# Performance work log

Hardware: AMD Instinct MI355X
Metric: run time of the kernel (lower is better)

Reference implementation:

```python
import jax, jax.numpy as jnp
import numpy as np

# Module dims (match init_kwargs)
D_IN = 1024
N_PRI = 2048
D_PRI = 16
N_CLS = 25
D_CLS = 16
ITERS = 3
B = 64
EPS = 1e-6


def layer_norm(x, g, b, eps=1e-5):
    m = x.mean(-1, keepdims=True)
    v = ((x - m) ** 2).mean(-1, keepdims=True)
    return (x - m) / jnp.sqrt(v + eps) * g + b


def setup_inputs() -> dict:
    key = jax.random.key(0)
    ks = jax.random.split(key, 6)
    s = lambda n: 1.0 / np.sqrt(n)
    return {
        "z": jax.random.normal(ks[0], (B, D_IN), jnp.float32),
        # to_primary: Linear(d_in, n_primary*d_primary)
        "w1": jax.random.normal(ks[1], (D_IN, N_PRI * D_PRI), jnp.float32) * s(D_IN),
        "b1": jnp.zeros((N_PRI * D_PRI,), jnp.float32),
        # primary_act: LayerNorm(d_in) -> Linear(d_in, n_primary) -> Sigmoid
        "ln1_g": jnp.ones((D_IN,), jnp.float32),
        "ln1_b": jnp.zeros((D_IN,), jnp.float32),
        "w2": jax.random.normal(ks[2], (D_IN, N_PRI), jnp.float32) * s(D_IN),
        "b2": jnp.zeros((N_PRI,), jnp.float32),
        # CapsuleFC transform + EM routing params
        "w_caps": jax.random.normal(ks[3], (N_PRI, D_PRI, N_CLS, D_CLS), jnp.float32) * s(D_PRI),
        "beta_u": jnp.zeros((N_CLS,), jnp.float32),
        "beta_a": jnp.zeros((N_CLS,), jnp.float32),
        # to_logits: LayerNorm(d_class) -> Linear(d_class, 1)
        "ln2_g": jnp.ones((D_CLS,), jnp.float32),
        "ln2_b": jnp.zeros((D_CLS,), jnp.float32),
        "w3": jax.random.normal(ks[4], (D_CLS, 1), jnp.float32) * s(D_CLS),
        "b3": jnp.zeros((1,), jnp.float32),
    }


def em_routing(V, a_in, beta_u, beta_a, n_iter):
    # V: (b, n_in, n_out, d) votes; a_in: (b, n_in) primary activations
    b, n, o, d = V.shape
    R = jnp.full((b, n, o), 1.0 / o, V.dtype)  # routing assignments
    lam = jnp.asarray(1.0, V.dtype)            # inverse temperature
    for _ in range(n_iter):
        # M-step: weighted mean/variance per output capsule
        r = R * a_in[:, :, None]                                  # (b,n,o)
        r_sum = r.sum(axis=1) + EPS                               # (b,o)
        mu = jnp.einsum('bno,bnod->bod', r, V) / r_sum[..., None]  # (b,o,d)
        diff2 = (V - mu[:, None]) ** 2                            # (b,n,o,d)
        sigma2 = jnp.einsum('bno,bnod->bod', r, diff2) / r_sum[..., None] + EPS
        cost = (beta_u[None, :, None] + 0.5 * jnp.log(sigma2)) * r_sum[..., None]
        a_out = jax.nn.sigmoid(lam * (beta_a[None, :] - cost.sum(-1)))  # (b,o)
        # E-step: Gaussian log-likelihood of each vote under each output capsule
        logp = (-0.5 * (diff2 / sigma2[:, None]).sum(-1)
                - 0.5 * jnp.log(sigma2).sum(-1)[:, None, :])      # (b,n,o)
        R = jax.nn.softmax(jnp.log(a_out + EPS)[:, None, :] + logp, axis=-1)
    return mu, a_out, R


def reference(z, w1, b1, ln1_g, ln1_b, w2, b2, w_caps, beta_u, beta_a,
              ln2_g, ln2_b, w3, b3):
    b = z.shape[0]
    # primary poses (no squash: use_squash_primary=False)
    primary_pose = (z @ w1 + b1).reshape(b, N_PRI, D_PRI)
    # primary activations
    primary_act = jnp.clip(jax.nn.sigmoid(layer_norm(z, ln1_g, ln1_b) @ w2 + b2), 0.0, 1.0)
    # votes: each primary capsule predicts each class capsule's pose
    V = jnp.einsum('bni,niod->bnod', primary_pose, w_caps)  # (B, N_PRI, N_CLS, D_CLS)
    class_pose, class_act, q = em_routing(V, primary_act, beta_u, beta_a, ITERS)
    logits = (layer_norm(class_pose, ln2_g, ln2_b) @ w3 + b3).squeeze(-1)  # (B, N_CLS)
    acts = jnp.linalg.norm(class_pose, axis=-1)                            # (B, N_CLS)
    return logits, acts, class_pose, q
```

## Files before the change

kernel.cpp:

```cpp
#include <hip/hip_runtime.h>
#include <hip/hip_bf16.h>
#include <cstdio>

#define B     64
#define DIN   1024
#define NPRI  2048
#define DPRI  16
#define NCLS  25
#define DCLS  16
#define EMEPS 1e-6f
#define LNEPS 1e-5f
#define KS2   8
#define NCHUNK_S 16

#define OFF_POSE 0
#define OFF_ZN   (OFF_POSE + NPRI*DPRI*B)
#define OFF_ACTT (OFF_ZN + B*DIN)
#define OFF_G2P  (OFF_ACTT + NPRI*B)
#define OFF_V    (OFF_G2P + KS2*NPRI*B)
#define V_FLOATS (NPRI*NCLS*B*DCLS/2)
#define OFF_R    (OFF_V + V_FLOATS)
#define R_FLOATS (NPRI*NCLS*B/2)
#define OFF_PART (OFF_R + R_FLOATS)
#define OFF_STAT (OFF_PART + NCLS*NCHUNK_S*33*B)
#define OFF_MU   (OFF_STAT + NCLS*33*B)
#define OFF_MI4  (OFF_MU + NCLS*DCLS*B)
#define OFF_BASE (OFF_MI4 + NCLS*8*B*4)
#define OFF_ZH   (OFF_BASE + NCLS*B)
#define WS_FLOATS (OFF_ZH + B*DIN/2)

typedef __attribute__((ext_vector_type(8))) _Float16 f16x8;
typedef __attribute__((ext_vector_type(4))) float f32x4;

__device__ __forceinline__ unsigned pack_f16(float a, float b) {
  union { _Float16 h[2]; unsigned u; } x;
  x.h[0] = (_Float16)a; x.h[1] = (_Float16)b;
  return x.u;
}
__device__ __forceinline__ float f16lo(unsigned u) {
  union { unsigned u; _Float16 h[2]; } x; x.u = u; return (float)x.h[0];
}
__device__ __forceinline__ float f16hi(unsigned u) {
  union { unsigned u; _Float16 h[2]; } x; x.u = u; return (float)x.h[1];
}
__device__ __forceinline__ unsigned short f16bits(float a) {
  union { _Float16 h; unsigned short u; } x; x.h = (_Float16)a; return x.u;
}
__device__ __forceinline__ float f16val(unsigned short u) {
  union { unsigned short u; _Float16 h; } x; x.u = u; return (float)x.h;
}

__global__ __launch_bounds__(256) void k_zh(const float* __restrict__ z,
                                            unsigned* __restrict__ zh) {
  int idx = blockIdx.x * 256 + threadIdx.x;
  float2 v = ((const float2*)z)[idx];
  zh[idx] = pack_f16(v.x, v.y);
}

__global__ __launch_bounds__(256) void k_ln(const float* __restrict__ z,
                                            const float* __restrict__ g,
                                            const float* __restrict__ bb,
                                            float* __restrict__ zn) {
  int row = blockIdx.x, t = threadIdx.x;
  const float* zr = z + row * DIN;
  float4 v = ((const float4*)zr)[t];
  float s  = v.x + v.y + v.z + v.w;
  float s2 = v.x*v.x + v.y*v.y + v.z*v.z + v.w*v.w;
  for (int off = 32; off; off >>= 1) {
    s  += __shfl_down(s, off);
    s2 += __shfl_down(s2, off);
  }
  __shared__ float ls[8];
  int wv = t >> 6, ln = t & 63;
  if (ln == 0) { ls[wv*2] = s; ls[wv*2+1] = s2; }
  __syncthreads();
  s  = ls[0] + ls[2] + ls[4] + ls[6];
  s2 = ls[1] + ls[3] + ls[5] + ls[7];
  float mean = s * (1.0f / DIN);
  float var  = s2 * (1.0f / DIN) - mean * mean;
  float inv  = 1.0f / sqrtf(var + LNEPS);
  float4 gg = ((const float4*)g)[t];
  float4 bv = ((const float4*)bb)[t];
  float4 o;
  o.x = (v.x - mean) * inv * gg.x + bv.x;
  o.y = (v.y - mean) * inv * gg.y + bv.y;
  o.z = (v.z - mean) * inv * gg.z + bv.z;
  o.w = (v.w - mean) * inv * gg.w + bv.w;
  ((float4*)(zn + row * DIN))[t] = o;
}

__global__ __launch_bounds__(512) void k_gemm1m(const unsigned* __restrict__ zh,
                                                const float* __restrict__ w1,
                                                const float* __restrict__ b1,
                                                float* __restrict__ poseT) {
  __shared__ __align__(16) unsigned bt[2][64 * 68];
  __shared__ __align__(16) unsigned zl[2][64 * 68];
  int t = threadIdx.x;
  int c0 = blockIdx.x * 64;
  int l = t & 63, w = t >> 6;
  int kh = w >> 2, cw = w & 3;
  int c15 = l & 15, kq = l >> 4;
  int h  = t >> 8;
  int th = t & 255;
  int s_kp = th >> 2;
  int s_q  = th & 3;

  f32x4 acc0 = {0,0,0,0}, acc1 = {0,0,0,0}, acc2 = {0,0,0,0}, acc3 = {0,0,0,0};

  for (int it = 0; it < 4; ++it) {
    int k0 = (h * 4 + it) * 128;
#pragma unroll
    for (int u = 0; u < 4; ++u) {
      int cq = s_q + 4 * u;
      const float* src0 = w1 + (size_t)(k0 + 2 * s_kp) * 32768 + c0 + cq * 4;
      float4 r0 = *(const float4*)src0;
      float4 r1 = *(const float4*)(src0 + 32768);
      unsigned* dst = &bt[h][(cq * 4) * 68 + s_kp];
      dst[0]   = pack_f16(r0.x, r1.x);
      dst[68]  = pack_f16(r0.y, r1.y);
      dst[136] = pack_f16(r0.z, r1.z);
      dst[204] = pack_f16(r0.w, r1.w);
    }
#pragma unroll
    for (int u = 0; u < 4; ++u) {
      int ku4 = s_q + 4 * u;
      uint4 v = *(const uint4*)&zh[(size_t)s_kp * 512 + (k0 >> 1) + ku4 * 4];
      *(uint4*)&zl[h][s_kp * 68 + ku4 * 4] = v;
    }
    __syncthreads();
#pragma unroll
    for (int ks = 0; ks < 4; ++ks) {
      union { uint4 u; f16x8 hh; } bf, a0, a1, a2, a3;
      bf.u = *(const uint4*)&bt[kh][(cw * 16 + c15) * 68 + ks * 16 + kq * 4];
      a0.u = *(const uint4*)&zl[kh][(c15)      * 68 + ks * 16 + kq * 4];
      a1.u = *(const uint4*)&zl[kh][(16 + c15) * 68 + ks * 16 + kq * 4];
      a2.u = *(const uint4*)&zl[kh][(32 + c15) * 68 + ks * 16 + kq * 4];
      a3.u = *(const uint4*)&zl[kh][(48 + c15) * 68 + ks * 16 + kq * 4];
      acc0 = __builtin_amdgcn_mfma_f32_16x16x32_f16(a0.hh, bf.hh, acc0, 0, 0, 0);
      acc1 = __builtin_amdgcn_mfma_f32_16x16x32_f16(a1.hh, bf.hh, acc1, 0, 0, 0);
      acc2 = __builtin_amdgcn_mfma_f32_16x16x32_f16(a2.hh, bf.hh, acc2, 0, 0, 0);
      acc3 = __builtin_amdgcn_mfma_f32_16x16x32_f16(a3.hh, bf.hh, acc3, 0, 0, 0);
    }
    __syncthreads();
  }

  float* red = (float*)&zl[0][0];
  if (kh == 1) {
    int cc = cw * 16 + c15;
    *(float4*)&red[cc * 68 + kq * 4]      = *(float4*)&acc0;
    *(float4*)&red[cc * 68 + 16 + kq * 4] = *(float4*)&acc1;
    *(float4*)&red[cc * 68 + 32 + kq * 4] = *(float4*)&acc2;
    *(float4*)&red[cc * 68 + 48 + kq * 4] = *(float4*)&acc3;
  }
  __syncthreads();
  if (kh == 0) {
    int cc = cw * 16 + c15;
    int c = c0 + cc;
    float bc = b1[c];
    float4 r0 = *(float4*)&red[cc * 68 + kq * 4];
    float4 r1 = *(float4*)&red[cc * 68 + 16 + kq * 4];
    float4 r2 = *(float4*)&red[cc * 68 + 32 + kq * 4];
    float4 r3 = *(float4*)&red[cc * 68 + 48 + kq * 4];
    float* pdst = poseT + (size_t)c * 64 + kq * 4;
    float4 o0 = {acc0[0] + r0.x + bc, acc0[1] + r0.y + bc, acc0[2] + r0.z + bc, acc0[3] + r0.w + bc};
    float4 o1 = {acc1[0] + r1.x + bc, acc1[1] + r1.y + bc, acc1[2] + r1.z + bc, acc1[3] + r1.w + bc};
    float4 o2 = {acc2[0] + r2.x + bc, acc2[1] + r2.y + bc, acc2[2] + r2.z + bc, acc2[3] + r2.w + bc};
    float4 o3 = {acc3[0] + r3.x + bc, acc3[1] + r3.y + bc, acc3[2] + r3.z + bc, acc3[3] + r3.w + bc};
    *(float4*)&pdst[0]  = o0;
    *(float4*)&pdst[16] = o1;
    *(float4*)&pdst[32] = o2;
    *(float4*)&pdst[48] = o3;
  }
}

__global__ __launch_bounds__(256, 2) void k_gemm2p(const float* __restrict__ zn,
                                                   const float* __restrict__ w2,
                                                   float* __restrict__ part) {
  __shared__ __align__(16) float znT[128 * 68];
  __shared__ __align__(16) float wl[128 * 68];
  int t = threadIdx.x;
  int c0 = blockIdx.x * 64;
  int k0 = blockIdx.y * 128;
  int zr_ = t >> 2, za = t & 3;
  int wk = t >> 1, wc = (t & 1) * 32;

#pragma unroll
  for (int jj = 0; jj < 4; ++jj) {
    int kb = za * 8 + jj * 32;
    const float* src = zn + zr_ * DIN + k0 + kb;
    float4 v0 = *(const float4*)src;
    float4 v1 = *(const float4*)(src + 4);
    znT[(kb+0)*68 + zr_] = v0.x; znT[(kb+1)*68 + zr_] = v0.y;
    znT[(kb+2)*68 + zr_] = v0.z; znT[(kb+3)*68 + zr_] = v0.w;
    znT[(kb+4)*68 + zr_] = v1.x; znT[(kb+5)*68 + zr_] = v1.y;
    znT[(kb+6)*68 + zr_] = v1.z; znT[(kb+7)*68 + zr_] = v1.w;
  }
  const float* wsrc = w2 + (size_t)(k0 + wk) * NPRI + c0 + wc;
#pragma unroll
  for (int j = 0; j < 8; ++j)
    *(float4*)&wl[wk * 68 + wc + j * 4] = *(const float4*)(wsrc + j * 4);
  __syncthreads();

  int r0 = (t >> 4) * 4, c0l = (t & 15) * 4;
  float acc[4][4];
#pragma unroll
  for (int j = 0; j < 4; ++j)
#pragma unroll
    for (int i = 0; i < 4; ++i) acc[j][i] = 0.f;

#pragma unroll 4
  for (int k = 0; k < 128; ++k) {
    float4 z4 = *(const float4*)&znT[k * 68 + r0];
    float4 w4 = *(const float4*)&wl[k * 68 + c0l];
    float zz[4] = {z4.x, z4.y, z4.z, z4.w};
    float ww[4] = {w4.x, w4.y, w4.z, w4.w};
#pragma unroll
    for (int j = 0; j < 4; ++j)
#pragma unroll
      for (int i = 0; i < 4; ++i) acc[j][i] += ww[j] * zz[i];
  }
  float* pdst = part + ((size_t)blockIdx.y * NPRI + c0 + c0l) * 64 + r0;
#pragma unroll
  for (int j = 0; j < 4; ++j) {
    float4 o = {acc[j][0], acc[j][1], acc[j][2], acc[j][3]};
    *(float4*)&pdst[j * 64] = o;
  }
}

__global__ __launch_bounds__(256) void k_gemm2r(const float* __restrict__ part,
                                                const float* __restrict__ b2,
                                                float* __restrict__ actt) {
  int idx = blockIdx.x * 256 + threadIdx.x;
  float4 s = {0.f, 0.f, 0.f, 0.f};
#pragma unroll
  for (int kz = 0; kz < KS2; ++kz) {
    float4 v = *(const float4*)&part[(size_t)kz * NPRI * 64 + idx * 4];
    s.x += v.x; s.y += v.y; s.z += v.z; s.w += v.w;
  }
  int c = (idx * 4) >> 6;
  float bc = b2[c];
  float4 o;
  o.x = fminf(fmaxf(1.0f / (1.0f + expf(-(s.x + bc))), 0.0f), 1.0f);
  o.y = fminf(fmaxf(1.0f / (1.0f + expf(-(s.y + bc))), 0.0f), 1.0f);
  o.z = fminf(fmaxf(1.0f / (1.0f + expf(-(s.z + bc))), 0.0f), 1.0f);
  o.w = fminf(fmaxf(1.0f / (1.0f + expf(-(s.w + bc))), 0.0f), 1.0f);
  *(float4*)&actt[idx * 4] = o;
}

__global__ __launch_bounds__(256) void k_votes(const float* __restrict__ poseT,
                                               const float* __restrict__ wcaps,
                                               unsigned* __restrict__ V) {
  __shared__ __align__(16) float wl[6400];
  __shared__ __align__(16) float pl[64 * 16];
  int n = blockIdx.x, t = threadIdx.x;
  const float* wsrc = wcaps + (size_t)n * 6400;
  for (int idx = t * 4; idx < 6400; idx += 1024)
    *(float4*)(wl + idx) = *(const float4*)(wsrc + idx);
  {
    float4 v = *(const float4*)(poseT + n * 1024 + t * 4);
    int i = (t * 4) >> 6, b = (t * 4) & 63;
    pl[(b+0)*16 + i] = v.x; pl[(b+1)*16 + i] = v.y;
    pl[(b+2)*16 + i] = v.z; pl[(b+3)*16 + i] = v.w;
  }
  __syncthreads();
  if (t >= 200) return;
  int o = t / 8, d0 = (t % 8) * 2;
  float w0[16], w1_[16];
#pragma unroll
  for (int i = 0; i < 16; ++i) {
    w0[i]  = wl[(i * 25 + o) * 16 + d0];
    w1_[i] = wl[(i * 25 + o) * 16 + d0 + 1];
  }
  unsigned* vd = V + (((size_t)n * 25 + o) * 64 * 16 + d0) / 2;
  for (int b = 0; b < 64; ++b) {
    const float* pb = &pl[b * 16];
    float a0 = 0.f, a1 = 0.f;
#pragma unroll
    for (int i = 0; i < 16; ++i) {
      float p = pb[i];
      a0 += p * w0[i];
      a1 += p * w1_[i];
    }
    vd[b * 8] = pack_f16(a0, a1);
  }
}

template <bool UNIFORM>
__global__ __launch_bounds__(256) void k_stats(const unsigned* __restrict__ V,
                                               const float* __restrict__ actt,
                                               const unsigned short* __restrict__ Rh,
                                               float* __restrict__ part) {
  int o = blockIdx.y;
  int t = threadIdx.x, b = t & 63, wv = t >> 6;
  float S0 = 0.f, S1[16], S2[16];
#pragma unroll
  for (int d = 0; d < 16; ++d) { S1[d] = 0.f; S2[d] = 0.f; }
  int n0 = blockIdx.x * 128 + wv * 32;
  for (int k = 0; k < 32; ++k) {
    int n = n0 + k;
    float a = actt[n * 64 + b];
    float r = UNIFORM ? a * (1.0f / 25.0f)
                      : f16val(Rh[((size_t)n * 25 + o) * 64 + b]) * a;
    const uint4* vp = (const uint4*)(V + (((size_t)n * 25 + o) * 64 + b) * 8);
    uint4 u0 = vp[0], u1 = vp[1];
    unsigned uu[8] = {u0.x, u0.y, u0.z, u0.w, u1.x, u1.y, u1.z, u1.w};
    S0 += r;
#pragma unroll
    for (int q = 0; q < 8; ++q) {
      float v0 = f16lo(uu[q]), v1 = f16hi(uu[q]);
      float t0 = r * v0, t1 = r * v1;
      S1[2*q]   += t0;          S1[2*q+1] += t1;
      S2[2*q]   += t0 * v0;     S2[2*q+1] += t1 * v1;
    }
  }
  __shared__ float red[4 * 33 * 64];
  red[(wv * 33 + 0) * 64 + b] = S0;
#pragma unroll
  for (int d = 0; d < 16; ++d) {
    red[(wv * 33 + 1 + d) * 64 + b]  = S1[d];
    red[(wv * 33 + 17 + d) * 64 + b] = S2[d];
  }
  __syncthreads();
  if (wv == 0) {
    for (int s = 0; s < 33; ++s) {
      float tot = red[s * 64 + b] + red[(33 + s) * 64 + b] +
                  red[(66 + s) * 64 + b] + red[(99 + s) * 64 + b];
      part[((o * NCHUNK_S + blockIdx.x) * 33 + s) * 64 + b] = tot;
    }
  }
}

__global__ __launch_bounds__(256) void k_reduce(const float* __restrict__ part,
                                                float* __restrict__ stats) {
  int o = blockIdx.x;
  for (int idx = threadIdx.x; idx < 33 * 64; idx += 256) {
    float s = 0.f;
#pragma unroll
    for (int c = 0; c < NCHUNK_S; ++c)
      s += part[(o * NCHUNK_S + c) * 33 * 64 + idx];
    stats[o * 33 * 64 + idx] = s;
  }
}

__global__ __launch_bounds__(64) void k_finish(const float* __restrict__ stats,
                                               const float* __restrict__ beta_u,
                                               const float* __restrict__ beta_a,
                                               float* __restrict__ mu,
                                               float* __restrict__ mi4,
                                               float* __restrict__ basew) {
  int o = blockIdx.x, b = threadIdx.x;
  const float* st = stats + o * 33 * 64;
  float s0 = st[b];
  float rs = s0 + EMEPS;
  float inv_rs = 1.0f / rs;
  float ldet = 0.f;
  float mloc[16], iloc[16];
#pragma unroll
  for (int d = 0; d < 16; ++d) {
    float s1 = st[(1 + d) * 64 + b];
    float s2 = st[(17 + d) * 64 + b];
    float m = s1 * inv_rs;
    float var = (s2 - 2.0f * m * s1 + m * m * s0) * inv_rs;
    float sg = fmaxf(var, 0.0f) + EMEPS;
    mloc[d] = m;
    iloc[d] = 1.0f / sg;
    mu[(o * 16 + d) * 64 + b] = m;
    ldet += logf(sg);
  }
#pragma unroll
  for (int q = 0; q < 8; ++q) {
    float4 v = {mloc[2*q], iloc[2*q], mloc[2*q+1], iloc[2*q+1]};
    *(float4*)&mi4[((o * 8 + q) * 64 + b) * 4] = v;
  }
  float cost = (16.0f * beta_u[o] + 0.5f * ldet) * rs;
  float x = beta_a[o] - cost;
  float a = 1.0f / (1.0f + expf(-x));
  basew[o * 64 + b] = logf(a + EMEPS) - 0.5f * ldet;
}

template <bool FINAL>
__global__ __launch_bounds__(256) void k_estep(const unsigned* __restrict__ V,
                                               const float* __restrict__ mi4,
                                               const float* __restrict__ basew,
                                               unsigned short* __restrict__ Rh,
                                               float* __restrict__ qout) {
  int t = threadIdx.x, b = t & 63, ng = t >> 6;
  int n = blockIdx.x * 4 + ng;
  float l[25];
  float mx = -1e30f;
#pragma unroll
  for (int o = 0; o < 25; ++o) {
    const uint4* vp = (const uint4*)(V + (((size_t)n * 25 + o) * 64 + b) * 8);
    uint4 u0 = vp[0], u1 = vp[1];
    unsigned uu[8] = {u0.x, u0.y, u0.z, u0.w, u1.x, u1.y, u1.z, u1.w};
    float acc = 0.f;
#pragma unroll
    for (int qq = 0; qq < 8; ++qq) {
      float4 mi = *(const float4*)&mi4[((o * 8 + qq) * 64 + b) * 4];
      float d0 = f16lo(uu[qq]) - mi.x;
      float d1 = f16hi(uu[qq]) - mi.z;
      acc += d0 * d0 * mi.y + d1 * d1 * mi.w;
    }
    l[o] = basew[o * 64 + b] - 0.5f * acc;
    mx = fmaxf(mx, l[o]);
  }
  float s = 0.f;
#pragma unroll
  for (int o = 0; o < 25; ++o) { l[o] = expf(l[o] - mx); s += l[o]; }
  float inv = 1.0f / s;
  if (FINAL) {
    float* qp = qout + ((size_t)b * NPRI + n) * 25;
#pragma unroll
    for (int o = 0; o < 25; ++o) qp[o] = l[o] * inv;
  } else {
#pragma unroll
    for (int o = 0; o < 25; ++o)
      Rh[((size_t)n * 25 + o) * 64 + b] = f16bits(l[o] * inv);
  }
}

__global__ __launch_bounds__(64) void k_out(const float* __restrict__ mu,
                                            const float* __restrict__ g2,
                                            const float* __restrict__ bb2,
                                            const float* __restrict__ w3,
                                            const float* __restrict__ b3,
                                            float* __restrict__ out) {
  int o = blockIdx.x, b = threadIdx.x;
  float m[16];
  float s = 0.f;
#pragma unroll
  for (int d = 0; d < 16; ++d) { m[d] = mu[(o * 16 + d) * 64 + b]; s += m[d]; }
  float mean = s * (1.0f / 16.0f);
  float var = 0.f;
#pragma unroll
  for (int d = 0; d < 16; ++d) { float dd = m[d] - mean; var += dd * dd; }
  var *= (1.0f / 16.0f);
  float inv = 1.0f / sqrtf(var + LNEPS);
  float logit = 0.f, nrm = 0.f;
#pragma unroll
  for (int d = 0; d < 16; ++d) {
    float nh = (m[d] - mean) * inv * g2[d] + bb2[d];
    logit += nh * w3[d];
    nrm += m[d] * m[d];
  }
  out[b * 25 + o] = logit + b3[0];
  out[1600 + b * 25 + o] = sqrtf(nrm);
  float* pp = out + 3200 + (b * 25 + o) * 16;
#pragma unroll
  for (int d = 0; d < 16; ++d) pp[d] = m[d];
}

extern "C" void kernel_launch(void* const* d_in, const int* in_sizes, int n_in,
                              void* d_out, int out_size, void* d_ws, size_t ws_size,
                              hipStream_t stream) {
  const float* z      = (const float*)d_in[0];
  const float* w1     = (const float*)d_in[1];
  const float* b1     = (const float*)d_in[2];
  const float* ln1g   = (const float*)d_in[3];
  const float* ln1b   = (const float*)d_in[4];
  const float* w2     = (const float*)d_in[5];
  const float* b2     = (const float*)d_in[6];
  const float* wcaps  = (const float*)d_in[7];
  const float* beta_u = (const float*)d_in[8];
  const float* beta_a = (const float*)d_in[9];
  const float* ln2g   = (const float*)d_in[10];
  const float* ln2b   = (const float*)d_in[11];
  const float* w3     = (const float*)d_in[12];
  const float* b3     = (const float*)d_in[13];

  if (ws_size < (size_t)WS_FLOATS * 4) {
    fprintf(stderr, "kernel_launch: ws too small: %zu < %zu bytes\n",
            ws_size, (size_t)WS_FLOATS * 4);
  }

  float* ws    = (float*)d_ws;
  float* out   = (float*)d_out;
  float* poseT = ws + OFF_POSE;
  float* zn    = ws + OFF_ZN;
  float* actt  = ws + OFF_ACTT;
  float* g2p   = ws + OFF_G2P;
  unsigned* V  = (unsigned*)(ws + OFF_V);
  unsigned short* Rh = (unsigned short*)(ws + OFF_R);
  float* part  = ws + OFF_PART;
  float* st    = ws + OFF_STAT;
  float* muw   = ws + OFF_MU;
  float* mi4   = ws + OFF_MI4;
  float* bse   = ws + OFF_BASE;
  unsigned* zh = (unsigned*)(ws + OFF_ZH);

  k_zh<<<128, 256, 0, stream>>>(z, zh);
  k_ln<<<64, 256, 0, stream>>>(z, ln1g, ln1b, zn);
  k_gemm1m<<<512, 512, 0, stream>>>(zh, w1, b1, poseT);
  k_gemm2p<<<dim3(32, KS2), 256, 0, stream>>>(zn, w2, g2p);
  k_gemm2r<<<128, 256, 0, stream>>>(g2p, b2, actt);
  k_votes<<<2048, 256, 0, stream>>>(poseT, wcaps, V);

  k_stats<true><<<dim3(NCHUNK_S, 25), 256, 0, stream>>>(V, actt, Rh, part);
  k_reduce<<<25, 256, 0, stream>>>(part, st);
  k_finish<<<25, 64, 0, stream>>>(st, beta_u, beta_a, muw, mi4, bse);

  for (int it = 0; it < 2; ++it) {
    k_estep<false><<<512, 256, 0, stream>>>(V, mi4, bse, Rh, nullptr);
    k_stats<false><<<dim3(NCHUNK_S, 25), 256, 0, stream>>>(V, actt, Rh, part);
    k_reduce<<<25, 256, 0, stream>>>(part, st);
    k_finish<<<25, 64, 0, stream>>>(st, beta_u, beta_a, muw, mi4, bse);
  }

  k_estep<true><<<512, 256, 0, stream>>>(V, mi4, bse, nullptr, out + 28800);
  k_out<<<25, 64, 0, stream>>>(muw, ln2g, ln2b, w3, b3, out);
}
```

Baseline: 357.9 us.

## Fuse small kernels, prefetch GEMM1 tiles in registers, double stats chunks

Merges the fp16 conversion of z into the layer-norm kernel, fuses the partial-sum reduction with the EM finish step, and folds the output head into the final finish kernel, which removes several tiny launches. The w1 GEMM now loads the next K tile into registers while the current tile is multiplied, to hide global-memory latency. The stats kernel uses twice as many chunks with shorter per-wave loops, for more parallelism. In exchange the reduce step reads more partial sums, and register pressure in the GEMM goes up.

```diff
diff --git a/kernel.cpp b/kernel.cpp
--- a/kernel.cpp
+++ b/kernel.cpp
@@ -11,7 +11,7 @@
 #define EMEPS 1e-6f
 #define LNEPS 1e-5f
 #define KS2   8
-#define NCHUNK_S 16
+#define NCH   32
 
 #define OFF_POSE 0
 #define OFF_ZN   (OFF_POSE + NPRI*DPRI*B)
@@ -22,8 +22,7 @@
 #define OFF_R    (OFF_V + V_FLOATS)
 #define R_FLOATS (NPRI*NCLS*B/2)
 #define OFF_PART (OFF_R + R_FLOATS)
-#define OFF_STAT (OFF_PART + NCLS*NCHUNK_S*33*B)
-#define OFF_MU   (OFF_STAT + NCLS*33*B)
+#define OFF_MU   (OFF_PART + NCLS*NCH*33*B)
 #define OFF_MI4  (OFF_MU + NCLS*DCLS*B)
 #define OFF_BASE (OFF_MI4 + NCLS*8*B*4)
 #define OFF_ZH   (OFF_BASE + NCLS*B)
@@ -50,20 +49,16 @@
   union { unsigned short u; _Float16 h; } x; x.u = u; return (float)x.h;
 }
 
-__global__ __launch_bounds__(256) void k_zh(const float* __restrict__ z,
-                                            unsigned* __restrict__ zh) {
-  int idx = blockIdx.x * 256 + threadIdx.x;
-  float2 v = ((const float2*)z)[idx];
-  zh[idx] = pack_f16(v.x, v.y);
-}
-
-__global__ __launch_bounds__(256) void k_ln(const float* __restrict__ z,
-                                            const float* __restrict__ g,
-                                            const float* __restrict__ bb,
-                                            float* __restrict__ zn) {
+__global__ __launch_bounds__(256) void k_lnzh(const float* __restrict__ z,
+                                              const float* __restrict__ g,
+                                              const float* __restrict__ bb,
+                                              float* __restrict__ zn,
+                                              unsigned* __restrict__ zh) {
   int row = blockIdx.x, t = threadIdx.x;
   const float* zr = z + row * DIN;
   float4 v = ((const float4*)zr)[t];
+  uint2 hz = {pack_f16(v.x, v.y), pack_f16(v.z, v.w)};
+  *(uint2*)&zh[row * 512 + t * 2] = hz;
   float s  = v.x + v.y + v.z + v.w;
   float s2 = v.x*v.x + v.y*v.y + v.z*v.z + v.w*v.w;
   for (int off = 32; off; off >>= 1) {
@@ -107,27 +102,43 @@
 
   f32x4 acc0 = {0,0,0,0}, acc1 = {0,0,0,0}, acc2 = {0,0,0,0}, acc3 = {0,0,0,0};
 
-  for (int it = 0; it < 4; ++it) {
-    int k0 = (h * 4 + it) * 128;
+  float4 wr0[4], wr1[4];
+  uint4  zr4[4];
+  {
+    int k0 = h * 512;
 #pragma unroll
     for (int u = 0; u < 4; ++u) {
       int cq = s_q + 4 * u;
       const float* src0 = w1 + (size_t)(k0 + 2 * s_kp) * 32768 + c0 + cq * 4;
-      float4 r0 = *(const float4*)src0;
-      float4 r1 = *(const float4*)(src0 + 32768);
+      wr0[u] = *(const float4*)src0;
+      wr1[u] = *(const float4*)(src0 + 32768);
+      zr4[u] = *(const uint4*)&zh[(size_t)s_kp * 512 + (k0 >> 1) + cq * 4];
+    }
+  }
+
+  for (int it = 0; it < 4; ++it) {
+#pragma unroll
+    for (int u = 0; u < 4; ++u) {
+      int cq = s_q + 4 * u;
       unsigned* dst = &bt[h][(cq * 4) * 68 + s_kp];
-      dst[0]   = pack_f16(r0.x, r1.x);
-      dst[68]  = pack_f16(r0.y, r1.y);
-      dst[136] = pack_f16(r0.z, r1.z);
-      dst[204] = pack_f16(r0.w, r1.w);
-    }
-#pragma unroll
-    for (int u = 0; u < 4; ++u) {
-      int ku4 = s_q + 4 * u;
-      uint4 v = *(const uint4*)&zh[(size_t)s_kp * 512 + (k0 >> 1) + ku4 * 4];
-      *(uint4*)&zl[h][s_kp * 68 + ku4 * 4] = v;
+      dst[0]   = pack_f16(wr0[u].x, wr1[u].x);
+      dst[68]  = pack_f16(wr0[u].y, wr1[u].y);
+      dst[136] = pack_f16(wr0[u].z, wr1[u].z);
+      dst[204] = pack_f16(wr0[u].w, wr1[u].w);
+      *(uint4*)&zl[h][s_kp * 68 + cq * 4] = zr4[u];
     }
     __syncthreads();
+    if (it < 3) {
+      int k0n = (h * 4 + it + 1) * 128;
+#pragma unroll
+      for (int u = 0; u < 4; ++u) {
+        int cq = s_q + 4 * u;
+        const float* src0 = w1 + (size_t)(k0n + 2 * s_kp) * 32768 + c0 + cq * 4;
+        wr0[u] = *(const float4*)src0;
+        wr1[u] = *(const float4*)(src0 + 32768);
+        zr4[u] = *(const uint4*)&zh[(size_t)s_kp * 512 + (k0n >> 1) + cq * 4];
+      }
+    }
 #pragma unroll
     for (int ks = 0; ks < 4; ++ks) {
       union { uint4 u; f16x8 hh; } bf, a0, a1, a2, a3;
@@ -295,8 +306,9 @@
   float S0 = 0.f, S1[16], S2[16];
 #pragma unroll
   for (int d = 0; d < 16; ++d) { S1[d] = 0.f; S2[d] = 0.f; }
-  int n0 = blockIdx.x * 128 + wv * 32;
-  for (int k = 0; k < 32; ++k) {
+  int n0 = blockIdx.x * 64 + wv * 16;
+#pragma unroll 2
+  for (int k = 0; k < 16; ++k) {
     int n = n0 + k;
     float a = actt[n * 64 + b];
     float r = UNIFORM ? a * (1.0f / 25.0f)
@@ -325,57 +337,85 @@
     for (int s = 0; s < 33; ++s) {
       float tot = red[s * 64 + b] + red[(33 + s) * 64 + b] +
                   red[(66 + s) * 64 + b] + red[(99 + s) * 64 + b];
-      part[((o * NCHUNK_S + blockIdx.x) * 33 + s) * 64 + b] = tot;
-    }
-  }
-}
-
-__global__ __launch_bounds__(256) void k_reduce(const float* __restrict__ part,
-                                                float* __restrict__ stats) {
-  int o = blockIdx.x;
-  for (int idx = threadIdx.x; idx < 33 * 64; idx += 256) {
+      part[((o * NCH + blockIdx.x) * 33 + s) * 64 + b] = tot;
+    }
+  }
+}
+
+template <bool FINAL>
+__global__ __launch_bounds__(256) void k_redfin(const float* __restrict__ part,
+                                                const float* __restrict__ beta_u,
+                                                const float* __restrict__ beta_a,
+                                                float* __restrict__ mu,
+                                                float* __restrict__ mi4,
+                                                float* __restrict__ basew,
+                                                const float* __restrict__ g2,
+                                                const float* __restrict__ bb2,
+                                                const float* __restrict__ w3,
+                                                const float* __restrict__ b3,
+                                                float* __restrict__ out) {
+  __shared__ float st[33 * 64];
+  int o = blockIdx.x, t = threadIdx.x;
+  for (int slot = t; slot < 33 * 64; slot += 256) {
     float s = 0.f;
-#pragma unroll
-    for (int c = 0; c < NCHUNK_S; ++c)
-      s += part[(o * NCHUNK_S + c) * 33 * 64 + idx];
-    stats[o * 33 * 64 + idx] = s;
-  }
-}
-
-__global__ __launch_bounds__(64) void k_finish(const float* __restrict__ stats,
-                                               const float* __restrict__ beta_u,
-                                               const float* __restrict__ beta_a,
-                                               float* __restrict__ mu,
-                                               float* __restrict__ mi4,
-                                               float* __restrict__ basew) {
-  int o = blockIdx.x, b = threadIdx.x;
-  const float* st = stats + o * 33 * 64;
-  float s0 = st[b];
-  float rs = s0 + EMEPS;
-  float inv_rs = 1.0f / rs;
-  float ldet = 0.f;
-  float mloc[16], iloc[16];
-#pragma unroll
-  for (int d = 0; d < 16; ++d) {
-    float s1 = st[(1 + d) * 64 + b];
-    float s2 = st[(17 + d) * 64 + b];
-    float m = s1 * inv_rs;
-    float var = (s2 - 2.0f * m * s1 + m * m * s0) * inv_rs;
-    float sg = fmaxf(var, 0.0f) + EMEPS;
-    mloc[d] = m;
-    iloc[d] = 1.0f / sg;
-    mu[(o * 16 + d) * 64 + b] = m;
-    ldet += logf(sg);
-  }
-#pragma unroll
-  for (int q = 0; q < 8; ++q) {
-    float4 v = {mloc[2*q], iloc[2*q], mloc[2*q+1], iloc[2*q+1]};
-    *(float4*)&mi4[((o * 8 + q) * 64 + b) * 4] = v;
-  }
-  float cost = (16.0f * beta_u[o] + 0.5f * ldet) * rs;
-  float x = beta_a[o] - cost;
-  float a = 1.0f / (1.0f + expf(-x));
-  basew[o * 64 + b] = logf(a + EMEPS) - 0.5f * ldet;
+    const float* pp = part + (size_t)o * NCH * 2112 + slot;
+    for (int c = 0; c < NCH; ++c) s += pp[(size_t)c * 2112];
+    st[slot] = s;
+  }
+  __syncthreads();
+  if (t < 64) {
+    int b = t;
+    float s0 = st[b];
+    float rsm = s0 + EMEPS;
+    float inv_rs = 1.0f / rsm;
+    float ldet = 0.f;
+    float mloc[16], iloc[16];
+#pragma unroll
+    for (int d = 0; d < 16; ++d) {
+      float s1 = st[(1 + d) * 64 + b];
+      float s2 = st[(17 + d) * 64 + b];
+      float m = s1 * inv_rs;
+      float var = (s2 - 2.0f * m * s1 + m * m * s0) * inv_rs;
+      float sg = fmaxf(var, 0.0f) + EMEPS;
+      mloc[d] = m;
+      iloc[d] = 1.0f / sg;
+      mu[(o * 16 + d) * 64 + b] = m;
+      ldet += logf(sg);
+    }
+#pragma unroll
+    for (int q = 0; q < 8; ++q) {
+      float4 v = {mloc[2*q], iloc[2*q], mloc[2*q+1], iloc[2*q+1]};
+      *(float4*)&mi4[((o * 8 + q) * 64 + b) * 4] = v;
+    }
+    float cost = (16.0f * beta_u[o] + 0.5f * ldet) * rsm;
+    float x = beta_a[o] - cost;
+    float a = 1.0f / (1.0f + expf(-x));
+    basew[o * 64 + b] = logf(a + EMEPS) - 0.5f * ldet;
+
+    if (FINAL) {
+      float sm = 0.f;
+#pragma unroll
+      for (int d = 0; d < 16; ++d) sm += mloc[d];
+      float mean = sm * (1.0f / 16.0f);
+      float var2 = 0.f;
+#pragma unroll
+      for (int d = 0; d < 16; ++d) { float dd = mloc[d] - mean; var2 += dd * dd; }
+      var2 *= (1.0f / 16.0f);
+      float inv2 = 1.0f / sqrtf(var2 + LNEPS);
+      float logit = 0.f, nrm = 0.f;
+#pragma unroll
+      for (int d = 0; d < 16; ++d) {
+        float nh = (mloc[d] - mean) * inv2 * g2[d] + bb2[d];
+        logit += nh * w3[d];
+        nrm += mloc[d] * mloc[d];
+      }
+      out[b * 25 + o] = logit + b3[0];
+      out[1600 + b * 25 + o] = sqrtf(nrm);
+      float* pp = out + 3200 + (b * 25 + o) * 16;
+#pragma unroll
+      for (int d = 0; d < 16; ++d) pp[d] = mloc[d];
+    }
+  }
 }
 
 template <bool FINAL>
@@ -417,37 +457,6 @@
     for (int o = 0; o < 25; ++o)
       Rh[((size_t)n * 25 + o) * 64 + b] = f16bits(l[o] * inv);
   }
-}
-
-__global__ __launch_bounds__(64) void k_out(const float* __restrict__ mu,
-                                            const float* __restrict__ g2,
-                                            const float* __restrict__ bb2,
-                                            const float* __restrict__ w3,
-                                            const float* __restrict__ b3,
-                                            float* __restrict__ out) {
-  int o = blockIdx.x, b = threadIdx.x;
-  float m[16];
-  float s = 0.f;
-#pragma unroll
-  for (int d = 0; d < 16; ++d) { m[d] = mu[(o * 16 + d) * 64 + b]; s += m[d]; }
-  float mean = s * (1.0f / 16.0f);
-  float var = 0.f;
-#pragma unroll
-  for (int d = 0; d < 16; ++d) { float dd = m[d] - mean; var += dd * dd; }
-  var *= (1.0f / 16.0f);
-  float inv = 1.0f / sqrtf(var + LNEPS);
-  float logit = 0.f, nrm = 0.f;
-#pragma unroll
-  for (int d = 0; d < 16; ++d) {
-    float nh = (m[d] - mean) * inv * g2[d] + bb2[d];
-    logit += nh * w3[d];
-    nrm += m[d] * m[d];
-  }
-  out[b * 25 + o] = logit + b3[0];
-  out[1600 + b * 25 + o] = sqrtf(nrm);
-  float* pp = out + 3200 + (b * 25 + o) * 16;
-#pragma unroll
-  for (int d = 0; d < 16; ++d) pp[d] = m[d];
 }
 
 extern "C" void kernel_launch(void* const* d_in, const int* in_sizes, int n_in,
@@ -482,30 +491,30 @@
   unsigned* V  = (unsigned*)(ws + OFF_V);
   unsigned short* Rh = (unsigned short*)(ws + OFF_R);
   float* part  = ws + OFF_PART;
-  float* st    = ws + OFF_STAT;
   float* muw   = ws + OFF_MU;
   float* mi4   = ws + OFF_MI4;
   float* bse   = ws + OFF_BASE;
   unsigned* zh = (unsigned*)(ws + OFF_ZH);
 
-  k_zh<<<128, 256, 0, stream>>>(z, zh);
-  k_ln<<<64, 256, 0, stream>>>(z, ln1g, ln1b, zn);
+  k_lnzh<<<64, 256, 0, stream>>>(z, ln1g, ln1b, zn, zh);
   k_gemm1m<<<512, 512, 0, stream>>>(zh, w1, b1, poseT);
   k_gemm2p<<<dim3(32, KS2), 256, 0, stream>>>(zn, w2, g2p);
   k_gemm2r<<<128, 256, 0, stream>>>(g2p, b2, actt);
   k_votes<<<2048, 256, 0, stream>>>(poseT, wcaps, V);
 
-  k_stats<true><<<dim3(NCHUNK_S, 25), 256, 0, stream>>>(V, actt, Rh, part);
-  k_reduce<<<25, 256, 0, stream>>>(part, st);
-  k_finish<<<25, 64, 0, stream>>>(st, beta_u, beta_a, muw, mi4, bse);
-
-  for (int it = 0; it < 2; ++it) {
-    k_estep<false><<<512, 256, 0, stream>>>(V, mi4, bse, Rh, nullptr);
-    k_stats<false><<<dim3(NCHUNK_S, 25), 256, 0, stream>>>(V, actt, Rh, part);
-    k_reduce<<<25, 256, 0, stream>>>(part, st);
-    k_finish<<<25, 64, 0, stream>>>(st, beta_u, beta_a, muw, mi4, bse);
-  }
+  k_stats<true><<<dim3(NCH, 25), 256, 0, stream>>>(V, actt, Rh, part);
+  k_redfin<false><<<25, 256, 0, stream>>>(part, beta_u, beta_a, muw, mi4, bse,
+                                          ln2g, ln2b, w3, b3, out);
+
+  k_estep<false><<<512, 256, 0, stream>>>(V, mi4, bse, Rh, nullptr);
+  k_stats<false><<<dim3(NCH, 25), 256, 0, stream>>>(V, actt, Rh, part);
+  k_redfin<false><<<25, 256, 0, stream>>>(part, beta_u, beta_a, muw, mi4, bse,
+                                          ln2g, ln2b, w3, b3, out);
+
+  k_estep<false><<<512, 256, 0, stream>>>(V, mi4, bse, Rh, nullptr);
+  k_stats<false><<<dim3(NCH, 25), 256, 0, stream>>>(V, actt, Rh, part);
+  k_redfin<true><<<25, 256, 0, stream>>>(part, beta_u, beta_a, muw, mi4, bse,
+                                         ln2g, ln2b, w3, b3, out);
 
   k_estep<true><<<512, 256, 0, stream>>>(V, mi4, bse, nullptr, out + 28800);
-  k_out<<<25, 64, 0, stream>>>(muw, ln2g, ln2b, w3, b3, out);
-}
+}
```

Measured after the change: 381.2 us. 6.5% more time.
